# Kernel optimization log

Hardware: AMD Instinct MI355X
Metric: run time of the kernel (lower is better)

The kernel has to match this reference:

```python
import jax, jax.numpy as jnp
import numpy as np

E = 8          # num_experts
DF = 512       # full_feature_dim
DE = 128       # expert_dim
H = 8          # num_heads
S = DF // E    # slice per expert = 64
GH = S // 4    # gate hidden = 16
HD = DE // H   # head_dim = 16
B, N = 2, 1024


def setup_inputs() -> dict:
    key = jax.random.key(0)
    ks = jax.random.split(key, 16)

    def xavier(k, shape):
        fan_out, fan_in = shape[-2], shape[-1]
        lim = jnp.sqrt(6.0 / (fan_in + fan_out))
        return jax.random.uniform(k, shape, jnp.float32, -lim, lim)

    return {
        "x": jax.random.normal(ks[0], (B, N, DF), jnp.float32),
        "fingerprints": jax.random.uniform(ks[1], (N,), jnp.float32),
        "ln_w": jnp.ones((DF,), jnp.float32),
        "ln_b": jnp.zeros((DF,), jnp.float32),
        "alpha": jnp.ones((E,), jnp.float32),                 # alpha_init per expert
        "Wg1": xavier(ks[2], (E, GH, S)),
        "bg1": jnp.zeros((E, GH), jnp.float32),
        "Wg2": xavier(ks[3], (E, 1, GH)),
        "bg2": jnp.zeros((E, 1), jnp.float32),
        "Wq": xavier(ks[4], (E, DE, S)),
        "Wk": xavier(ks[5], (E, DE, S)),
        "Wv": xavier(ks[6], (E, DE, S)),
        "temp": jnp.asarray(0.5, jnp.float32),
        "Wf": xavier(ks[7], (DF, DE)),
        "bf": jnp.zeros((DF,), jnp.float32),
    }


def _layernorm(x, w, b, eps=1e-5):
    mu = x.mean(-1, keepdims=True)
    var = ((x - mu) ** 2).mean(-1, keepdims=True)
    return (x - mu) * jax.lax.rsqrt(var + eps) * w + b


def reference(x, fingerprints, ln_w, ln_b, alpha, Wg1, bg1, Wg2, bg2,
              Wq, Wk, Wv, temp, Wf, bf):
    b, n, _ = x.shape
    xn = _layernorm(x, ln_w, ln_b)

    # slice features per expert: [E, B, N, S]
    f = jnp.transpose(xn.reshape(b, n, E, S), (2, 0, 1, 3))

    # Cantor bin masks [E, N] (last expert inclusive upper edge)
    edges = jnp.arange(E, dtype=fingerprints.dtype) / E
    lo = fingerprints[None, :] >= edges[:, None]
    hi_excl = fingerprints[None, :] < (edges[:, None] + 1.0 / E)
    hi_incl = fingerprints[None, :] <= (edges[:, None] + 1.0 / E)
    hi = jnp.where((jnp.arange(E) == E - 1)[:, None], hi_incl, hi_excl)
    m = (lo & hi).astype(f.dtype)  # [E, N]

    # per-expert alpha gate: Linear-GELU-Linear-Sigmoid
    g = jnp.einsum("ebns,ehs->ebnh", f, Wg1) + bg1[:, None, None, :]
    g = jax.nn.gelu(g, approximate=False)
    g = jnp.einsum("ebnh,eoh->ebno", g, Wg2) + bg2[:, None, None, :]
    g = jax.nn.sigmoid(g)                                    # [E,B,N,1]
    aw = jax.nn.sigmoid(alpha)[:, None, None, None]
    f = f * (g * aw + (1.0 - aw))

    # QKV projections (no bias): [E, B, N, DE]
    Q = jnp.einsum("ebns,eds->ebnd", f, Wq)
    K = jnp.einsum("ebns,eds->ebnd", f, Wk)
    V = jnp.einsum("ebns,eds->ebnd", f, Wv)

    # heads: [E, B, H, N, HD]
    def heads(t):
        return jnp.transpose(t.reshape(E, b, n, H, HD), (0, 1, 3, 2, 4))
    Qh, Kh, Vh = heads(Q), heads(K), heads(V)

    scale = jnp.sqrt(jnp.asarray(HD, f.dtype)) * jnp.abs(temp)
    scores = jnp.einsum("ebhqd,ebhkd->ebhqk", Qh, Kh) / scale
    scores = scores + (1.0 - m)[:, None, None, None, :] * (-1e9)  # mask keys
    attn = jax.nn.softmax(scores, axis=-1)
    out = jnp.einsum("ebhqk,ebhkd->ebhqd", attn, Vh)
    out = jnp.transpose(out, (0, 1, 3, 2, 4)).reshape(E, b, n, DE)

    # masked weighted combine across experts
    w = m[:, None, :, None]                                  # [E,1,N,1]
    fused = (out * w).sum(0) / jnp.clip(w.sum(0), 1.0)        # [B,N,DE]

    proj = fused @ Wf.T + bf                                  # [B,N,DF]
    return x + proj
```

## Files before the change

### kernel.cpp

```cpp
#include <hip/hip_runtime.h>
#include <math.h>

#define E 8
#define DF 512
#define DE 128
#define H 8
#define S 64
#define GH 16
#define HD 16
#define B 2
#define NTOK 1024
#define KMAX 256

__device__ __forceinline__ float wave_sum(float v) {
#pragma unroll
    for (int m = 32; m; m >>= 1) v += __shfl_xor(v, m, 64);
    return v;
}

__global__ __launch_bounds__(256) void k_fg(
    const float* __restrict__ Wf, const float* __restrict__ fp,
    const float* __restrict__ x,
    const float* __restrict__ lnw, const float* __restrict__ lnb,
    const float* __restrict__ alpha,
    const float* __restrict__ Wg1, const float* __restrict__ bg1,
    const float* __restrict__ Wg2, const float* __restrict__ bg2,
    float* __restrict__ WfT, float* __restrict__ fg) {
    __shared__ __align__(16) float sh[64][65];
    int bid = blockIdx.x, tid = threadIdx.x;
    if (bid < 16) {
        int rt = bid >> 1, ct2 = bid & 1;
        const float* in = Wf + (size_t)rt * 64 * DE + ct2 * 64;
        float* outp = WfT + (size_t)ct2 * 64 * DF + rt * 64;
        int cc = tid & 63, r0 = tid >> 6;
        for (int r = r0; r < 64; r += 4) sh[r][cc] = in[(size_t)r * DE + cc];
        __syncthreads();
        for (int c2 = r0; c2 < 64; c2 += 4)
            outp[(size_t)c2 * DF + cc] = sh[cc][c2];
        return;
    }
    float (*fsh)[64] = (float(*)[64])sh;
    int wave = tid >> 6, lane = tid & 63;
    int t = (bid - 16) * 4 + wave;
    int n = t & (NTOK - 1);
    const float* xr = x + (size_t)t * DF;
    float4 a  = *(const float4*)(xr + lane * 8);
    float4 b4 = *(const float4*)(xr + lane * 8 + 4);
    float s  = a.x + a.y + a.z + a.w + b4.x + b4.y + b4.z + b4.w;
    float ss = a.x*a.x + a.y*a.y + a.z*a.z + a.w*a.w
             + b4.x*b4.x + b4.y*b4.y + b4.z*b4.z + b4.w*b4.w;
    s = wave_sum(s);
    ss = wave_sum(ss);
    float mu  = s * (1.0f / DF);
    float var = ss * (1.0f / DF) - mu * mu;
    float rs  = rsqrtf(var + 1e-5f);
    int e = (int)(fp[n] * 8.0f);
    e = e > 7 ? 7 : e;
    float f = (xr[e * 64 + lane] - mu) * rs * lnw[e * 64 + lane]
            + lnb[e * 64 + lane];
    fsh[wave][lane] = f;
    __syncthreads();
    int hh = lane & 15, sb = (lane >> 4) * 16;
    const float* wg1 = Wg1 + ((size_t)e * GH + hh) * S;
    float g1p = 0.f;
#pragma unroll
    for (int si = 0; si < 16; si++) g1p += fsh[wave][sb + si] * wg1[sb + si];
    g1p += __shfl_xor(g1p, 16, 64);
    g1p += __shfl_xor(g1p, 32, 64);
    float g1 = g1p + bg1[e * GH + hh];
    g1 = 0.5f * g1 * (1.0f + erff(g1 * 0.70710678118654752f));
    float part = g1 * Wg2[e * GH + hh];
    part += __shfl_xor(part, 1, 64);
    part += __shfl_xor(part, 2, 64);
    part += __shfl_xor(part, 4, 64);
    part += __shfl_xor(part, 8, 64);
    float g2 = part + bg2[e];
    float gate = 1.0f / (1.0f + __expf(-g2));
    float aw = 1.0f / (1.0f + __expf(-alpha[e]));
    float gm = gate * aw + (1.0f - aw);
    fg[(size_t)t * S + lane] = f * gm;
}

__global__ __launch_bounds__(256) void k_attn3(
    const float* __restrict__ Wq, const float* __restrict__ Wk,
    const float* __restrict__ Wv, const float* __restrict__ fp,
    const float* __restrict__ fg, const float* __restrict__ temp,
    float* __restrict__ F) {
    union UA {
        struct { float Wsh[3][16][68]; float Qsh[64][16]; } bw;
        float part[4][64][18];
    };
    __shared__ __align__(16) UA ua;
    __shared__ __align__(16) float Ksh[KMAX][16];
    __shared__ __align__(16) float Vsh[KMAX][16];
    __shared__ unsigned short Lsh[KMAX];
    __shared__ int wcnt[4];
    int bid = blockIdx.x;
    int qt = bid & 3, h = (bid >> 2) & 7, e = (bid >> 5) & 7, b = bid >> 8;
    int tid = threadIdx.x, w = tid >> 6, lane = tid & 63;

    unsigned long long mm[4];
    int cw = 0;
#pragma unroll
    for (int j = 0; j < 4; j++) {
        int n = w * 256 + j * 64 + lane;
        int ee = (int)(fp[n] * 8.0f); ee = ee > 7 ? 7 : ee;
        mm[j] = __ballot(ee == e);
        cw += __popcll(mm[j]);
    }
    if (lane == 0) wcnt[w] = cw;
    __syncthreads();
    int base = 0, c = 0;
#pragma unroll
    for (int j = 0; j < 4; j++) { int cj = wcnt[j]; c += cj; if (j < w) base += cj; }
    int qb = qt * 64;
    if (qb >= c) return;
    unsigned long long ltm = (1ull << lane) - 1ull;
    int off = base;
#pragma unroll
    for (int j = 0; j < 4; j++) {
        if ((mm[j] >> lane) & 1ull) {
            int p = off + __popcll(mm[j] & ltm);
            if (p < KMAX) Lsh[p] = (unsigned short)(w * 256 + j * 64 + lane);
        }
        off += __popcll(mm[j]);
    }
    if (c > KMAX) c = KMAX;

    for (int idx = tid; idx < 3 * HD * S; idx += 256) {
        int mat = idx >> 10, r = idx & 1023, d = r >> 6, s = r & 63;
        const float* W = (mat == 0) ? Wq : (mat == 1) ? Wk : Wv;
        ua.bw.Wsh[mat][d][s] = W[((size_t)(e * DE + h * HD + d)) * S + s];
    }
    __syncthreads();

    int q4 = tid & 3;
    for (int ii = tid >> 2; ii < c; ii += 64) {
        const float* fr = fg + (size_t)(b * NTOK + (int)Lsh[ii]) * S;
        float aq[4] = {0,0,0,0}, ak[4] = {0,0,0,0}, av[4] = {0,0,0,0};
#pragma unroll
        for (int s4 = 0; s4 < 16; s4++) {
            float4 fv = ((const float4*)fr)[s4];
#pragma unroll
            for (int dd = 0; dd < 4; dd++) {
                float4 wq = *(const float4*)&ua.bw.Wsh[0][q4 * 4 + dd][s4 * 4];
                float4 wk = *(const float4*)&ua.bw.Wsh[1][q4 * 4 + dd][s4 * 4];
                float4 wv = *(const float4*)&ua.bw.Wsh[2][q4 * 4 + dd][s4 * 4];
                aq[dd] += fv.x*wq.x + fv.y*wq.y + fv.z*wq.z + fv.w*wq.w;
                ak[dd] += fv.x*wk.x + fv.y*wk.y + fv.z*wk.z + fv.w*wk.w;
                av[dd] += fv.x*wv.x + fv.y*wv.y + fv.z*wv.z + fv.w*wv.w;
            }
        }
        *(float4*)&Ksh[ii][q4 * 4] = make_float4(ak[0], ak[1], ak[2], ak[3]);
        *(float4*)&Vsh[ii][q4 * 4] = make_float4(av[0], av[1], av[2], av[3]);
        if (ii >= qb && ii < qb + 64)
            *(float4*)&ua.bw.Qsh[ii - qb][q4 * 4] = make_float4(aq[0], aq[1], aq[2], aq[3]);
    }
    __syncthreads();

    float inv_scale = 1.0f / (4.0f * fabsf(temp[0]));
    int qi = qb + lane;
    bool valid = qi < c;
    int qrow = (valid ? qi : c - 1) - qb;
    float q[16];
#pragma unroll
    for (int d4 = 0; d4 < 4; d4++) {
        float4 qv = ((const float4*)ua.bw.Qsh[qrow])[d4];
        q[4*d4]   = qv.x * inv_scale; q[4*d4+1] = qv.y * inv_scale;
        q[4*d4+2] = qv.z * inv_scale; q[4*d4+3] = qv.w * inv_scale;
    }
    __syncthreads();

    int ck = (c + 3) >> 2;
    int k0 = w * ck, k1 = min(c, k0 + ck);
    float m = -1e30f, l = 0.f;
    float acc[16];
#pragma unroll
    for (int d = 0; d < 16; d++) acc[d] = 0.f;

    for (int i = k0; i < k1; i++) {
        const float4* kr = (const float4*)Ksh[i];
        float4 ka = kr[0], kb = kr[1], kc = kr[2], kd = kr[3];
        float sc = q[0]*ka.x + q[1]*ka.y + q[2]*ka.z + q[3]*ka.w
                 + q[4]*kb.x + q[5]*kb.y + q[6]*kb.z + q[7]*kb.w
                 + q[8]*kc.x + q[9]*kc.y + q[10]*kc.z + q[11]*kc.w
                 + q[12]*kd.x + q[13]*kd.y + q[14]*kd.z + q[15]*kd.w;
        if (__any(sc - m > 8.0f)) {
            float mn = fmaxf(m, sc);
            float r = __expf(m - mn);
            l *= r;
#pragma unroll
            for (int d = 0; d < 16; d++) acc[d] *= r;
            m = mn;
        }
        float p = __expf(sc - m);
        l += p;
        const float4* vr = (const float4*)Vsh[i];
        float4 va = vr[0], vb = vr[1], vc = vr[2], vd = vr[3];
        acc[0] += p*va.x; acc[1] += p*va.y; acc[2] += p*va.z; acc[3] += p*va.w;
        acc[4] += p*vb.x; acc[5] += p*vb.y; acc[6] += p*vb.z; acc[7] += p*vb.w;
        acc[8] += p*vc.x; acc[9] += p*vc.y; acc[10]+= p*vc.z; acc[11]+= p*vc.w;
        acc[12]+= p*vd.x; acc[13]+= p*vd.y; acc[14]+= p*vd.z; acc[15]+= p*vd.w;
    }

    float* pp = ua.part[w][lane];
    pp[0] = m; pp[1] = l;
#pragma unroll
    for (int d = 0; d < 16; d++) pp[2 + d] = acc[d];
    __syncthreads();

    if (w == 0) {
        float M = ua.part[0][lane][0];
        M = fmaxf(M, ua.part[1][lane][0]);
        M = fmaxf(M, ua.part[2][lane][0]);
        M = fmaxf(M, ua.part[3][lane][0]);
        float Lt = 0.f;
        float o[16];
#pragma unroll
        for (int d = 0; d < 16; d++) o[d] = 0.f;
#pragma unroll
        for (int ww = 0; ww < 4; ww++) {
            const float* qq = ua.part[ww][lane];
            float r = __expf(qq[0] - M);
            Lt += qq[1] * r;
#pragma unroll
            for (int d = 0; d < 16; d++) o[d] += qq[2 + d] * r;
        }
        if (valid) {
            float il = 1.0f / Lt;
            float* op = F + (size_t)(b * NTOK + (int)Lsh[qi]) * DE + h * HD;
#pragma unroll
            for (int d4 = 0; d4 < 4; d4++)
                ((float4*)op)[d4] = make_float4(o[4*d4]*il, o[4*d4+1]*il,
                                                o[4*d4+2]*il, o[4*d4+3]*il);
        }
    }
}

__global__ __launch_bounds__(512) void k_proj(
    const float* __restrict__ x, const float* __restrict__ F,
    const float* __restrict__ WfT, const float* __restrict__ bf,
    float* __restrict__ out) {
    __shared__ float fr[8][DE];
    __shared__ float pp[8][DF];
    int t0 = blockIdx.x * 8;
    int tid = threadIdx.x;
    if (tid < 256) ((float4*)fr)[tid] = ((const float4*)(F + (size_t)t0 * DE))[tid];
    __syncthreads();
    int kh = tid >> 8, tt = tid & 255;
    float acc0[8], acc1[8];
#pragma unroll
    for (int tk = 0; tk < 8; tk++) { acc0[tk] = 0.f; acc1[tk] = 0.f; }
    int kb = kh * 64;
#pragma unroll 4
    for (int k = kb; k < kb + 64; k++) {
        float w0 = WfT[(size_t)k * DF + tt];
        float w1 = WfT[(size_t)k * DF + tt + 256];
#pragma unroll
        for (int tk = 0; tk < 8; tk++) {
            float fv = fr[tk][k];
            acc0[tk] += fv * w0;
            acc1[tk] += fv * w1;
        }
    }
    if (kh == 1) {
#pragma unroll
        for (int tk = 0; tk < 8; tk++) {
            pp[tk][tt]       = acc0[tk];
            pp[tk][tt + 256] = acc1[tk];
        }
    }
    __syncthreads();
    if (kh == 0) {
        float b0 = bf[tt], b1 = bf[tt + 256];
#pragma unroll
        for (int tk = 0; tk < 8; tk++) {
            size_t rb = (size_t)(t0 + tk) * DF;
            out[rb + tt]       = x[rb + tt]       + b0 + acc0[tk] + pp[tk][tt];
            out[rb + tt + 256] = x[rb + tt + 256] + b1 + acc1[tk] + pp[tk][tt + 256];
        }
    }
}

extern "C" void kernel_launch(void* const* d_in, const int* in_sizes, int n_in,
                              void* d_out, int out_size, void* d_ws, size_t ws_size,
                              hipStream_t stream) {
    (void)in_sizes; (void)n_in; (void)out_size; (void)ws_size;
    const float* x     = (const float*)d_in[0];
    const float* fp    = (const float*)d_in[1];
    const float* lnw   = (const float*)d_in[2];
    const float* lnb   = (const float*)d_in[3];
    const float* alpha = (const float*)d_in[4];
    const float* Wg1   = (const float*)d_in[5];
    const float* bg1   = (const float*)d_in[6];
    const float* Wg2   = (const float*)d_in[7];
    const float* bg2   = (const float*)d_in[8];
    const float* Wq    = (const float*)d_in[9];
    const float* Wk    = (const float*)d_in[10];
    const float* Wv    = (const float*)d_in[11];
    const float* temp  = (const float*)d_in[12];
    const float* Wf    = (const float*)d_in[13];
    const float* bf    = (const float*)d_in[14];
    float* out = (float*)d_out;

    char* ws = (char*)d_ws;
    float* fg  = (float*)ws;
    float* Fb  = fg + (size_t)B * NTOK * S;
    float* WfT = Fb + (size_t)B * NTOK * DE;

    hipLaunchKernelGGL(k_fg, dim3(528), dim3(256), 0, stream,
                       Wf, fp, x, lnw, lnb, alpha, Wg1, bg1, Wg2, bg2, WfT, fg);
    hipLaunchKernelGGL(k_attn3, dim3(B * E * H * 4), dim3(256), 0, stream,
                       Wq, Wk, Wv, fp, fg, temp, Fb);
    hipLaunchKernelGGL(k_proj, dim3(B * NTOK / 8), dim3(512), 0, stream,
                       x, Fb, WfT, bf, out);
}
```

Baseline: 42.80 us.

## Split attention keys across two blocks and merge partial softmax in projection

Each attention block now handles half of the expert's keys instead of all of them. It covers a strided set of query tiles and projects only Q for those queries plus K/V for its key half. Unnormalized partial outputs with their running max and sum go to a workspace, and the projection kernel merges the two halves before the GEMM. This is meant to remove redundant K/V projection and put more blocks to work, at the cost of extra partial-result traffic and merge arithmetic.

```diff
diff --git a/kernel.cpp b/kernel.cpp
--- a/kernel.cpp
+++ b/kernel.cpp
@@ -81,22 +81,27 @@
     fg[(size_t)t * S + lane] = f * gm;
 }
 
-__global__ __launch_bounds__(256) void k_attn3(
+struct AU {
+    union {
+        float Wsh[3][16][68];
+        float mrg[4][64][18];
+    } u;
+    float Ksh[128][16];
+    float Vsh[128][16];
+    float Qsh[128][16];
+    unsigned short Lsh[KMAX];
+    int wcnt[4];
+};
+
+__global__ __launch_bounds__(256) void k_attn6(
     const float* __restrict__ Wq, const float* __restrict__ Wk,
     const float* __restrict__ Wv, const float* __restrict__ fp,
     const float* __restrict__ fg, const float* __restrict__ temp,
-    float* __restrict__ F) {
-    union UA {
-        struct { float Wsh[3][16][68]; float Qsh[64][16]; } bw;
-        float part[4][64][18];
-    };
-    __shared__ __align__(16) UA ua;
-    __shared__ __align__(16) float Ksh[KMAX][16];
-    __shared__ __align__(16) float Vsh[KMAX][16];
-    __shared__ unsigned short Lsh[KMAX];
-    __shared__ int wcnt[4];
+    float* __restrict__ Pb) {
+    __shared__ __align__(16) AU sm;
     int bid = blockIdx.x;
-    int qt = bid & 3, h = (bid >> 2) & 7, e = (bid >> 5) & 7, b = bid >> 8;
+    int kh = bid & 1, qt = (bid >> 1) & 1;
+    int h = (bid >> 2) & 7, e = (bid >> 5) & 7, b = bid >> 8;
     int tid = threadIdx.x, w = tid >> 6, lane = tid & 63;
 
     unsigned long long mm[4];
@@ -108,144 +113,169 @@
         mm[j] = __ballot(ee == e);
         cw += __popcll(mm[j]);
     }
-    if (lane == 0) wcnt[w] = cw;
+    if (lane == 0) sm.wcnt[w] = cw;
     __syncthreads();
     int base = 0, c = 0;
 #pragma unroll
-    for (int j = 0; j < 4; j++) { int cj = wcnt[j]; c += cj; if (j < w) base += cj; }
-    int qb = qt * 64;
-    if (qb >= c) return;
+    for (int j = 0; j < 4; j++) { int cj = sm.wcnt[j]; c += cj; if (j < w) base += cj; }
+    if (qt * 64 >= c) return;
     unsigned long long ltm = (1ull << lane) - 1ull;
     int off = base;
 #pragma unroll
     for (int j = 0; j < 4; j++) {
         if ((mm[j] >> lane) & 1ull) {
             int p = off + __popcll(mm[j] & ltm);
-            if (p < KMAX) Lsh[p] = (unsigned short)(w * 256 + j * 64 + lane);
+            if (p < KMAX) sm.Lsh[p] = (unsigned short)(w * 256 + j * 64 + lane);
         }
         off += __popcll(mm[j]);
     }
     if (c > KMAX) c = KMAX;
+    int ch0 = (c + 1) >> 1;
+    int kstart = kh * ch0;
+    int kend = min(c, kstart + ch0);
+    int nk = kend - kstart;
 
     for (int idx = tid; idx < 3 * HD * S; idx += 256) {
         int mat = idx >> 10, r = idx & 1023, d = r >> 6, s = r & 63;
         const float* W = (mat == 0) ? Wq : (mat == 1) ? Wk : Wv;
-        ua.bw.Wsh[mat][d][s] = W[((size_t)(e * DE + h * HD + d)) * S + s];
+        sm.u.Wsh[mat][d][s] = W[((size_t)(e * DE + h * HD + d)) * S + s];
     }
     __syncthreads();
 
     int q4 = tid & 3;
-    for (int ii = tid >> 2; ii < c; ii += 64) {
-        const float* fr = fg + (size_t)(b * NTOK + (int)Lsh[ii]) * S;
-        float aq[4] = {0,0,0,0}, ak[4] = {0,0,0,0}, av[4] = {0,0,0,0};
+    for (int jj = tid >> 2; jj < 128; jj += 64) {
+        int qi = qt * 64 + ((jj >> 6) << 7) + (jj & 63);
+        bool vq = qi < c;
+        const float* fr = fg + (size_t)(b * NTOK + (int)sm.Lsh[vq ? qi : 0]) * S;
+        float aq[4] = {0, 0, 0, 0};
 #pragma unroll
         for (int s4 = 0; s4 < 16; s4++) {
             float4 fv = ((const float4*)fr)[s4];
 #pragma unroll
             for (int dd = 0; dd < 4; dd++) {
-                float4 wq = *(const float4*)&ua.bw.Wsh[0][q4 * 4 + dd][s4 * 4];
-                float4 wk = *(const float4*)&ua.bw.Wsh[1][q4 * 4 + dd][s4 * 4];
-                float4 wv = *(const float4*)&ua.bw.Wsh[2][q4 * 4 + dd][s4 * 4];
+                float4 wq = *(const float4*)&sm.u.Wsh[0][q4 * 4 + dd][s4 * 4];
                 aq[dd] += fv.x*wq.x + fv.y*wq.y + fv.z*wq.z + fv.w*wq.w;
+            }
+        }
+        if (vq) *(float4*)&sm.Qsh[jj][q4 * 4] = make_float4(aq[0], aq[1], aq[2], aq[3]);
+    }
+    for (int jj = tid >> 2; jj < nk; jj += 64) {
+        const float* fr = fg + (size_t)(b * NTOK + (int)sm.Lsh[kstart + jj]) * S;
+        float ak[4] = {0,0,0,0}, av[4] = {0,0,0,0};
+#pragma unroll
+        for (int s4 = 0; s4 < 16; s4++) {
+            float4 fv = ((const float4*)fr)[s4];
+#pragma unroll
+            for (int dd = 0; dd < 4; dd++) {
+                float4 wk = *(const float4*)&sm.u.Wsh[1][q4 * 4 + dd][s4 * 4];
+                float4 wv = *(const float4*)&sm.u.Wsh[2][q4 * 4 + dd][s4 * 4];
                 ak[dd] += fv.x*wk.x + fv.y*wk.y + fv.z*wk.z + fv.w*wk.w;
                 av[dd] += fv.x*wv.x + fv.y*wv.y + fv.z*wv.z + fv.w*wv.w;
             }
         }
-        *(float4*)&Ksh[ii][q4 * 4] = make_float4(ak[0], ak[1], ak[2], ak[3]);
-        *(float4*)&Vsh[ii][q4 * 4] = make_float4(av[0], av[1], av[2], av[3]);
-        if (ii >= qb && ii < qb + 64)
-            *(float4*)&ua.bw.Qsh[ii - qb][q4 * 4] = make_float4(aq[0], aq[1], aq[2], aq[3]);
+        *(float4*)&sm.Ksh[jj][q4 * 4] = make_float4(ak[0], ak[1], ak[2], ak[3]);
+        *(float4*)&sm.Vsh[jj][q4 * 4] = make_float4(av[0], av[1], av[2], av[3]);
     }
     __syncthreads();
 
     float inv_scale = 1.0f / (4.0f * fabsf(temp[0]));
-    int qi = qb + lane;
-    bool valid = qi < c;
-    int qrow = (valid ? qi : c - 1) - qb;
-    float q[16];
-#pragma unroll
-    for (int d4 = 0; d4 < 4; d4++) {
-        float4 qv = ((const float4*)ua.bw.Qsh[qrow])[d4];
-        q[4*d4]   = qv.x * inv_scale; q[4*d4+1] = qv.y * inv_scale;
-        q[4*d4+2] = qv.z * inv_scale; q[4*d4+3] = qv.w * inv_scale;
-    }
-    __syncthreads();
-
-    int ck = (c + 3) >> 2;
-    int k0 = w * ck, k1 = min(c, k0 + ck);
-    float m = -1e30f, l = 0.f;
-    float acc[16];
-#pragma unroll
-    for (int d = 0; d < 16; d++) acc[d] = 0.f;
-
-    for (int i = k0; i < k1; i++) {
-        const float4* kr = (const float4*)Ksh[i];
-        float4 ka = kr[0], kb = kr[1], kc = kr[2], kd = kr[3];
-        float sc = q[0]*ka.x + q[1]*ka.y + q[2]*ka.z + q[3]*ka.w
-                 + q[4]*kb.x + q[5]*kb.y + q[6]*kb.z + q[7]*kb.w
-                 + q[8]*kc.x + q[9]*kc.y + q[10]*kc.z + q[11]*kc.w
-                 + q[12]*kd.x + q[13]*kd.y + q[14]*kd.z + q[15]*kd.w;
-        if (__any(sc - m > 8.0f)) {
-            float mn = fmaxf(m, sc);
-            float r = __expf(m - mn);
-            l *= r;
-#pragma unroll
-            for (int d = 0; d < 16; d++) acc[d] *= r;
-            m = mn;
-        }
-        float p = __expf(sc - m);
-        l += p;
-        const float4* vr = (const float4*)Vsh[i];
-        float4 va = vr[0], vb = vr[1], vc = vr[2], vd = vr[3];
-        acc[0] += p*va.x; acc[1] += p*va.y; acc[2] += p*va.z; acc[3] += p*va.w;
-        acc[4] += p*vb.x; acc[5] += p*vb.y; acc[6] += p*vb.z; acc[7] += p*vb.w;
-        acc[8] += p*vc.x; acc[9] += p*vc.y; acc[10]+= p*vc.z; acc[11]+= p*vc.w;
-        acc[12]+= p*vd.x; acc[13]+= p*vd.y; acc[14]+= p*vd.z; acc[15]+= p*vd.w;
-    }
-
-    float* pp = ua.part[w][lane];
-    pp[0] = m; pp[1] = l;
-#pragma unroll
-    for (int d = 0; d < 16; d++) pp[2 + d] = acc[d];
-    __syncthreads();
-
-    if (w == 0) {
-        float M = ua.part[0][lane][0];
-        M = fmaxf(M, ua.part[1][lane][0]);
-        M = fmaxf(M, ua.part[2][lane][0]);
-        M = fmaxf(M, ua.part[3][lane][0]);
-        float Lt = 0.f;
-        float o[16];
-#pragma unroll
-        for (int d = 0; d < 16; d++) o[d] = 0.f;
-#pragma unroll
-        for (int ww = 0; ww < 4; ww++) {
-            const float* qq = ua.part[ww][lane];
-            float r = __expf(qq[0] - M);
-            Lt += qq[1] * r;
-#pragma unroll
-            for (int d = 0; d < 16; d++) o[d] += qq[2 + d] * r;
-        }
-        if (valid) {
-            float il = 1.0f / Lt;
-            float* op = F + (size_t)(b * NTOK + (int)Lsh[qi]) * DE + h * HD;
-#pragma unroll
-            for (int d4 = 0; d4 < 4; d4++)
-                ((float4*)op)[d4] = make_float4(o[4*d4]*il, o[4*d4+1]*il,
-                                                o[4*d4+2]*il, o[4*d4+3]*il);
-        }
+    int cl16 = (nk + 3) >> 2;
+    int myk0 = w * cl16, myk1 = min(nk, myk0 + cl16);
+
+    for (int pass = 0; qt * 64 + pass * 128 < c; pass++) {
+        int qb0 = qt * 64 + pass * 128;
+        int qi = qb0 + lane;
+        bool valid = qi < c;
+        int qloc = pass * 64 + (valid ? lane : 0);
+        float q[16];
+#pragma unroll
+        for (int d4 = 0; d4 < 4; d4++) {
+            float4 qv = *(const float4*)&sm.Qsh[qloc][d4 * 4];
+            q[4*d4]   = qv.x * inv_scale; q[4*d4+1] = qv.y * inv_scale;
+            q[4*d4+2] = qv.z * inv_scale; q[4*d4+3] = qv.w * inv_scale;
+        }
+        float m = -1e30f, l = 0.f;
+        float acc[16];
+#pragma unroll
+        for (int dd = 0; dd < 16; dd++) acc[dd] = 0.f;
+
+        for (int i = myk0; i < myk1; i++) {
+            const float4* kr = (const float4*)sm.Ksh[i];
+            float4 ka = kr[0], kb = kr[1], kc = kr[2], kd = kr[3];
+            float sc = q[0]*ka.x + q[1]*ka.y + q[2]*ka.z + q[3]*ka.w
+                     + q[4]*kb.x + q[5]*kb.y + q[6]*kb.z + q[7]*kb.w
+                     + q[8]*kc.x + q[9]*kc.y + q[10]*kc.z + q[11]*kc.w
+                     + q[12]*kd.x + q[13]*kd.y + q[14]*kd.z + q[15]*kd.w;
+            if (__any(sc - m > 8.0f)) {
+                float mn = fmaxf(m, sc);
+                float r = __expf(m - mn);
+                l *= r;
+#pragma unroll
+                for (int dd = 0; dd < 16; dd++) acc[dd] *= r;
+                m = mn;
+            }
+            float p = __expf(sc - m);
+            l += p;
+            const float4* vr = (const float4*)sm.Vsh[i];
+            float4 va = vr[0], vb = vr[1], vc = vr[2], vd = vr[3];
+            acc[0] += p*va.x; acc[1] += p*va.y; acc[2] += p*va.z; acc[3] += p*va.w;
+            acc[4] += p*vb.x; acc[5] += p*vb.y; acc[6] += p*vb.z; acc[7] += p*vb.w;
+            acc[8] += p*vc.x; acc[9] += p*vc.y; acc[10]+= p*vc.z; acc[11]+= p*vc.w;
+            acc[12]+= p*vd.x; acc[13]+= p*vd.y; acc[14]+= p*vd.z; acc[15]+= p*vd.w;
+        }
+        float* pp = sm.u.mrg[w][lane];
+        pp[0] = m; pp[1] = l;
+#pragma unroll
+        for (int dd = 0; dd < 16; dd++) pp[2 + dd] = acc[dd];
+        __syncthreads();
+        if (w == 0) {
+            float M = sm.u.mrg[0][lane][0];
+            M = fmaxf(M, sm.u.mrg[1][lane][0]);
+            M = fmaxf(M, sm.u.mrg[2][lane][0]);
+            M = fmaxf(M, sm.u.mrg[3][lane][0]);
+            float Lt = 0.f;
+            float o[16];
+#pragma unroll
+            for (int dd = 0; dd < 16; dd++) o[dd] = 0.f;
+#pragma unroll
+            for (int ww = 0; ww < 4; ww++) {
+                const float* qq = sm.u.mrg[ww][lane];
+                float r = __expf(qq[0] - M);
+                Lt += qq[1] * r;
+#pragma unroll
+                for (int dd = 0; dd < 16; dd++) o[dd] += qq[2 + dd] * r;
+            }
+            if (valid) {
+                int n = (int)sm.Lsh[qi];
+                float* op = Pb + ((size_t)((b * NTOK + n) * H + h) * 2 + kh) * 20;
+#pragma unroll
+                for (int dd = 0; dd < 16; dd++) op[dd] = o[dd];
+                op[16] = M; op[17] = Lt;
+            }
+        }
+        __syncthreads();
     }
 }
 
 __global__ __launch_bounds__(512) void k_proj(
-    const float* __restrict__ x, const float* __restrict__ F,
+    const float* __restrict__ x, const float* __restrict__ Pb,
     const float* __restrict__ WfT, const float* __restrict__ bf,
     float* __restrict__ out) {
     __shared__ float fr[8][DE];
     __shared__ float pp[8][DF];
     int t0 = blockIdx.x * 8;
     int tid = threadIdx.x;
-    if (tid < 256) ((float4*)fr)[tid] = ((const float4*)(F + (size_t)t0 * DE))[tid];
+    if (tid < 64) {
+        int tok = tid >> 3, hh = tid & 7;
+        const float* pB = Pb + (size_t)((t0 + tok) * H + hh) * 2 * 20;
+        float m0 = pB[16], l0 = pB[17], m1 = pB[36], l1 = pB[37];
+        float M = fmaxf(m0, m1);
+        float e0 = __expf(m0 - M), e1 = __expf(m1 - M);
+        float il = 1.0f / (l0 * e0 + l1 * e1);
+#pragma unroll
+        for (int d = 0; d < 16; d++)
+            fr[tok][hh * 16 + d] = (pB[d] * e0 + pB[20 + d] * e1) * il;
+    }
     __syncthreads();
     int kh = tid >> 8, tt = tid & 255;
     float acc0[8], acc1[8];
@@ -305,13 +335,13 @@
 
     char* ws = (char*)d_ws;
     float* fg  = (float*)ws;
-    float* Fb  = fg + (size_t)B * NTOK * S;
-    float* WfT = Fb + (size_t)B * NTOK * DE;
+    float* Pb  = fg + (size_t)B * NTOK * S;
+    float* WfT = Pb + (size_t)B * NTOK * H * 2 * 20;
 
     hipLaunchKernelGGL(k_fg, dim3(528), dim3(256), 0, stream,
                        Wf, fp, x, lnw, lnb, alpha, Wg1, bg1, Wg2, bg2, WfT, fg);
-    hipLaunchKernelGGL(k_attn3, dim3(B * E * H * 4), dim3(256), 0, stream,
-                       Wq, Wk, Wv, fp, fg, temp, Fb);
+    hipLaunchKernelGGL(k_attn6, dim3(B * E * H * 4), dim3(256), 0, stream,
+                       Wq, Wk, Wv, fp, fg, temp, Pb);
     hipLaunchKernelGGL(k_proj, dim3(B * NTOK / 8), dim3(512), 0, stream,
-                       x, Fb, WfT, bf, out);
-}
+                       x, Pb, WfT, bf, out);
+}
```

Result: slower. 43.99 us (+2.8%).
